# Performance work log

Hardware: AMD Instinct MI355X
Metric: run time of the kernel (lower is better)

The kernel has to match this reference:

```python
import jax, jax.numpy as jnp
import numpy as np
from jax import lax

B = 64
HW = 72           # high-res grid hardcoded in the layer
LOW = 9           # 72 / stride 8
C = 3
N_ITERS = 200     # self._iterations
W_SCALE = 0.01    # keeps the FISTA operator contractive with random weights
DN = ('NHWC', 'HWIO', 'NHWC')


def setup_inputs() -> dict:
    key = jax.random.key(0)
    k1, k2, k3, k4 = jax.random.split(key, 4)
    x = jax.random.normal(k1, (B, LOW, LOW, C), jnp.float32)
    lam = jax.random.uniform(k2, (B,), jnp.float32)            # per-sample threshold
    w_conv = jax.random.normal(k3, (40, 40, C, C), jnp.float32) * W_SCALE  # Conv2D kernel
    b_conv = jnp.zeros((C,), jnp.float32)
    w_ct = jax.random.normal(k4, (5, 5, C, C), jnp.float32) * W_SCALE      # Conv2DTranspose kernel
    b_ct = jnp.zeros((C,), jnp.float32)
    return {"x": x, "lam": lam, "w_conv": w_conv, "b_conv": b_conv,
            "w_ct": w_ct, "b_ct": b_ct}


def reference(x, lam, w_conv, b_conv, w_ct, b_ct):
    lam4 = lam[:, None, None, None]  # (B,1,1,1) per-sample soft-threshold

    def A(y):  # Conv2D(3,(40,40),strides=8,'same'): (B,72,72,3)->(B,9,9,3)
        return lax.conv_general_dilated(y, w_conv, (8, 8), 'SAME',
                                        dimension_numbers=DN) + b_conv

    def At(r):  # Conv2DTranspose(3,(5,5),strides=8,'same'): (B,9,9,3)->(B,72,72,3)
        return lax.conv_transpose(r, w_ct, (8, 8), 'SAME',
                                  dimension_numbers=DN) + b_ct

    def softthresh(w):
        return jax.nn.relu(w - lam4) - jax.nn.relu(-w - lam4)

    def step(carry, _):
        y_tmp, y_last, t = carry
        re = At(x - A(y_tmp))
        w = y_tmp - re                      # mu = 1.0
        y_new = softthresh(w)
        t_n = (1.0 + jnp.sqrt(1.0 + 4.0 * t * t)) / 2.0
        y_tmp_next = y_new + (t - 1.0) / t_n * (y_new - y_last)
        return (y_tmp_next, y_new, t_n), None

    z = jnp.zeros((x.shape[0], HW, HW, C), x.dtype)
    init = (z, z, jnp.float32(1.0))
    (_, y_new, _), _ = lax.scan(step, init, None, length=N_ITERS)
    return y_new
```

## Files before the change

kernel.cpp:

```cpp
#include <hip/hip_runtime.h>
#include <math.h>


#define ITERS 200
#define THREADS 576
#define WGOFF 0
#define WCTOFF 19200
#define APOFF 19800
#define CNTOFF 144256
#define LY 0
#define LYL 3888
#define LA 7776
#define LXS 8020
#define LWG 8264
#define LWCT 14664
#define LT 15264
#define SMEMF 20608

typedef float f32x2 __attribute__((ext_vector_type(2)));

template <int CTRL>
__device__ __forceinline__ float dpp_add(float x) {
  int moved = __builtin_amdgcn_update_dpp(0, __float_as_int(x), CTRL, 0xF, 0xF, true);
  return x + __int_as_float(moved);
}

__global__ void k0_init(const float* __restrict__ w_conv,
                        const float* __restrict__ w_ct,
                        float* __restrict__ ws) {
  const int i = blockIdx.x * 256 + threadIdx.x;
  if (i < 19200) {
    const int lane = i & 63;
    const int rest = i >> 6;
    const int g = rest / 75;
    const int tc = rest - 75 * g;
    const int t = tc / 3;
    const int co = tc - 3 * t;
    const int th = t / 5;
    const int tw = t - 5 * th;
    const int q = lane >> 4;
    const int pl = lane & 15;
    float v = 0.f;
    if (q < 3) {
      const int p = g * 16 + pl;
      const int ph = p >> 3;
      const int pw = p & 7;
      v = w_conv[(((8 * th + ph) * 40 + (8 * tw + pw)) * 3 + q) * 3 + co];
    }
    ws[WGOFF + i] = v;
  }
  if (i < 600) {
    const int c = i / 200;
    const int rem = i - 200 * c;
    float v = 0.f;
    if (rem < 192) {
      const int ci = rem >> 6;
      const int p = rem & 63;
      const int rh = p >> 3;
      const int rw = p & 7;
      if (rh < 5 && rw < 5) v = w_ct[(((4 - rh) * 5 + (4 - rw)) * 3 + ci) * 3 + c];
    }
    ws[WCTOFF + i] = v;
  }
  if (i < 4096) ((int*)ws)[CNTOFF + i] = 0;
}

__global__ __launch_bounds__(THREADS) void fista_split(
    float* __restrict__ ws,
    const float* __restrict__ x, const float* __restrict__ lam,
    const float* __restrict__ b_conv, const float* __restrict__ b_ct,
    float* __restrict__ out) {
  __shared__ __align__(16) float smem[SMEMF];
  const int tid = threadIdx.x;
  const int blk = blockIdx.x;
  const int n = blk & 63;
  const int g = blk >> 6;
  const int lane = tid & 63;
  const int wid = tid >> 6;
  const int q = lane >> 4;
  const int pl = lane & 15;
  const int ylane = ((q < 3) ? q : 2) * 16 + pl;
  const int oh = (wid == 0) ? 0 : (wid == 1) ? 4 : (wid == 4) ? 8
               : (wid == 8) ? 1 : wid;

  int* __restrict__ cnt = (int*)ws + CNTOFF + n * 64;
  const float lam_n = lam[n];
  const float bcv = b_conv[tid % 3];
  const float bct0 = b_ct[0], bct1 = b_ct[1], bct2 = b_ct[2];

  for (int i = tid; i < SMEMF; i += THREADS) smem[i] = 0.f;
  __syncthreads();
  for (int i = tid; i < 4800; i += THREADS) {
    const int lane_i = i & 63;
    const int tc = i >> 6;
    const int t_i = tc / 3;
    const int co_i = tc - 3 * t_i;
    smem[LWG + (t_i * 64 + lane_i) * 4 + co_i] = ws[WGOFF + g * 4800 + i];
  }
  for (int i = tid; i < 600; i += THREADS) smem[LWCT + i] = ws[WCTOFF + i];
  if (tid < 243) smem[LXS + tid] = x[n * 243 + tid];
  __syncthreads();

  const int idx3 = tid >> 1;
  const int cell = idx3 / 3;
  const int c = idx3 - 3 * cell;
  const int cb = 3 * cell;
  const int plb = (tid & 1) * 8;
  const int pb = g * 16 + plb;

  float t = 1.0f;
#pragma unroll 1
  for (int iter = 0; iter < ITERS; ++iter) {
    {
      f32x2 a01[9];
      float a2[9];
#pragma unroll
      for (int k = 0; k < 9; ++k) { a01[k].x = 0.f; a01[k].y = 0.f; a2[k] = 0.f; }

#pragma unroll
      for (int th = 0; th < 5; ++th) {
        const int r = oh + th - 2;
        if (r >= 0 && r <= 8) {
          f32x2 y2[9];
#pragma unroll
          for (int wc = 0; wc < 9; ++wc) {
            const float yv = smem[LY + r * 432 + wc * 48 + ylane];
            y2[wc].x = yv; y2[wc].y = yv;
          }

#pragma unroll
          for (int tw = 0; tw < 5; ++tw) {
            const float4 wv =
                *(const float4*)&smem[LWG + ((th * 5 + tw) * 64 + lane) * 4];
            f32x2 w01; w01.x = wv.x; w01.y = wv.y;
#pragma unroll
            for (int ow = 0; ow < 9; ++ow) {
              const int col = ow + tw - 2;
              if (col >= 0 && col <= 8) {
                a01[ow] += y2[col] * w01;
                a2[ow]  += y2[col].x * wv.z;
              }
            }
          }
        }
      }

      float s4[27];
#pragma unroll
      for (int k = 0; k < 27; ++k) {
        const int ow = k / 3, co = k - 3 * ow;
        const float av = (co == 0) ? a01[ow].x : (co == 1) ? a01[ow].y : a2[ow];
        const float s1 = dpp_add<0x111>(av);
        s4[k] = dpp_add<0x112>(s1);
      }
      {
        float* Tw = &smem[LT + wid * 540];
        if ((lane & 3) == 3) {
          const int m = lane >> 2;
#pragma unroll
          for (int k = 0; k < 27; ++k) Tw[k * 20 + m] = s4[k];
        }
        asm volatile("s_waitcnt lgkmcnt(0)" ::: "memory");
        if (lane < 27) {
          const float4* Tr = (const float4*)&Tw[lane * 20];
          const float4 p0 = Tr[0];
          const float4 p1 = Tr[1];
          const float4 p2 = Tr[2];
          const float4 p3 = Tr[3];
          const float s01 = (p0.x + p0.y) + (p0.z + p0.w);
          const float s23 = (p1.x + p1.y) + (p1.z + p1.w);
          const float s45 = (p2.x + p2.y) + (p2.z + p2.w);
          const float s67 = (p3.x + p3.y) + (p3.z + p3.w);
          const float s = (s01 + s23) + (s45 + s67);
          float* ap = ws + APOFF + ((((iter & 1) * 64 + n) * 4 + g) * 243)
                      + oh * 27 + lane;
          __hip_atomic_store(ap, s, __ATOMIC_RELAXED, __HIP_MEMORY_SCOPE_AGENT);
        }
      }
    }

    float4 py0 = {}, py1 = {}, pq0 = {}, pq1 = {};
    float4 w0a = {}, w0b = {}, w1a = {}, w1b = {}, w2a = {}, w2b = {};
    if (tid < 486) {
      float4* lyv  = (float4*)&smem[LY];
      float4* lylv = (float4*)&smem[LYL];
      py0 = lyv[2 * tid];  py1 = lyv[2 * tid + 1];
      pq0 = lylv[2 * tid]; pq1 = lylv[2 * tid + 1];
      w0a = *(const float4*)&smem[LWCT + c * 200 +   0 + pb];
      w0b = *(const float4*)&smem[LWCT + c * 200 +   4 + pb];
      w1a = *(const float4*)&smem[LWCT + c * 200 +  64 + pb];
      w1b = *(const float4*)&smem[LWCT + c * 200 +  68 + pb];
      w2a = *(const float4*)&smem[LWCT + c * 200 + 128 + pb];
      w2b = *(const float4*)&smem[LWCT + c * 200 + 132 + pb];
    }

    __syncthreads();
    if (tid == 0) {
      __hip_atomic_fetch_add(cnt, 1, __ATOMIC_RELAXED, __HIP_MEMORY_SCOPE_AGENT);
      const int target = 4 * (iter + 1);
      while (__hip_atomic_load(cnt, __ATOMIC_RELAXED, __HIP_MEMORY_SCOPE_AGENT)
             < target)
        __builtin_amdgcn_s_sleep(1);
    }
    __syncthreads();

    if (tid < 243) {
      const float* ap = ws + APOFF + ((iter & 1) * 64 + n) * 972;
      const float a0 = __hip_atomic_load(ap + tid, __ATOMIC_RELAXED,
                                         __HIP_MEMORY_SCOPE_AGENT);
      const float a1 = __hip_atomic_load(ap + 243 + tid, __ATOMIC_RELAXED,
                                         __HIP_MEMORY_SCOPE_AGENT);
      const float a2v = __hip_atomic_load(ap + 486 + tid, __ATOMIC_RELAXED,
                                          __HIP_MEMORY_SCOPE_AGENT);
      const float a3 = __hip_atomic_load(ap + 729 + tid, __ATOMIC_RELAXED,
                                         __HIP_MEMORY_SCOPE_AGENT);
      smem[LA + tid] = smem[LXS + tid] - (a0 + a1 + a2v + a3 + bcv);
    }
    __syncthreads();

    const float tn = (1.0f + sqrtf(1.0f + 4.0f * t * t)) * 0.5f;
    const float beta = (t - 1.0f) / tn;
    t = tn;

    const bool lastit = (iter == ITERS - 1);
    if (tid < 486) {
      const float r0  = smem[LA + cb + 0];
      const float r1  = smem[LA + cb + 1];
      const float r2v = smem[LA + cb + 2];
      const float bct = (c == 0) ? bct0 : ((c == 1) ? bct1 : bct2);

      const float wct0[8] = {w0a.x, w0a.y, w0a.z, w0a.w, w0b.x, w0b.y, w0b.z, w0b.w};
      const float wct1[8] = {w1a.x, w1a.y, w1a.z, w1a.w, w1b.x, w1b.y, w1b.z, w1b.w};
      const float wct2[8] = {w2a.x, w2a.y, w2a.z, w2a.w, w2b.x, w2b.y, w2b.z, w2b.w};
      const float yv[8]   = {py0.x, py0.y, py0.z, py0.w, py1.x, py1.y, py1.z, py1.w};
      float yn[8];
#pragma unroll
      for (int j = 0; j < 8; ++j) {
        const float re = bct + r0 * wct0[j] + r1 * wct1[j] + r2v * wct2[j];
        const float wvv = yv[j] - re;
        yn[j] = fmaxf(wvv - lam_n, 0.f) - fmaxf(-wvv - lam_n, 0.f);
      }

      float4* lyv  = (float4*)&smem[LY];
      float4* lylv = (float4*)&smem[LYL];
      if (!lastit) {
        const float ylv[8] = {pq0.x, pq0.y, pq0.z, pq0.w, pq1.x, pq1.y, pq1.z, pq1.w};
        float4 s0, s1, m0, m1;
        s0.x = yn[0]; s0.y = yn[1]; s0.z = yn[2]; s0.w = yn[3];
        s1.x = yn[4]; s1.y = yn[5]; s1.z = yn[6]; s1.w = yn[7];
        m0.x = yn[0] + beta * (yn[0] - ylv[0]);
        m0.y = yn[1] + beta * (yn[1] - ylv[1]);
        m0.z = yn[2] + beta * (yn[2] - ylv[2]);
        m0.w = yn[3] + beta * (yn[3] - ylv[3]);
        m1.x = yn[4] + beta * (yn[4] - ylv[4]);
        m1.y = yn[5] + beta * (yn[5] - ylv[5]);
        m1.z = yn[6] + beta * (yn[6] - ylv[6]);
        m1.w = yn[7] + beta * (yn[7] - ylv[7]);
        lylv[2 * tid] = s0; lylv[2 * tid + 1] = s1;
        lyv[2 * tid]  = m0; lyv[2 * tid + 1]  = m1;
      } else {
        const int part = pb >> 3;
        const int qh = cell / 9;
        const int qw = cell - 9 * qh;
        const int ih = 8 * qh + part;
        float* op = out + ((n * 72 + ih) * 72 + 8 * qw) * 3 + c;
#pragma unroll
        for (int j = 0; j < 8; ++j) op[3 * j] = yn[j];
      }
    }
    __syncthreads();
  }
}

extern "C" void kernel_launch(void* const* d_in, const int* in_sizes, int n_in,
                              void* d_out, int out_size, void* d_ws, size_t ws_size,
                              hipStream_t stream) {
  const float* x      = (const float*)d_in[0];
  const float* lam    = (const float*)d_in[1];
  const float* w_conv = (const float*)d_in[2];
  const float* b_conv = (const float*)d_in[3];
  const float* w_ct   = (const float*)d_in[4];
  const float* b_ct   = (const float*)d_in[5];
  float* out = (float*)d_out;
  float* ws  = (float*)d_ws;

  hipLaunchKernelGGL(k0_init, dim3(80), dim3(256), 0, stream, w_conv, w_ct, ws);
  hipLaunchKernelGGL(fista_split, dim3(256), dim3(THREADS), 0, stream,
                     ws, x, lam, b_conv, b_ct, out);
}
```

Baseline: 955.5 us.

## Replace counter barrier with sentinel-flagged partial buffers and split y smem layout

```diff
diff --git a/kernel.cpp b/kernel.cpp
--- a/kernel.cpp
+++ b/kernel.cpp
@@ -4,10 +4,11 @@
 
 #define ITERS 200
 #define THREADS 576
+#define SENTU 0x7FC0DEADu
 #define WGOFF 0
 #define WCTOFF 19200
 #define APOFF 19800
-#define CNTOFF 144256
+#define CNTOFF 268632
 #define LY 0
 #define LYL 3888
 #define LA 7776
@@ -62,6 +63,8 @@
     }
     ws[WCTOFF + i] = v;
   }
+  for (int j = i; j < 248832; j += 80 * 256)
+    ((unsigned*)ws)[APOFF + j] = SENTU;
   if (i < 4096) ((int*)ws)[CNTOFF + i] = 0;
 }
 
@@ -80,6 +83,7 @@
   const int q = lane >> 4;
   const int pl = lane & 15;
   const int ylane = ((q < 3) ? q : 2) * 16 + pl;
+  const int ylane2 = ((ylane >> 2) & 1) * 1944 + (ylane >> 3) * 4 + (ylane & 3);
   const int oh = (wid == 0) ? 0 : (wid == 1) ? 4 : (wid == 4) ? 8
                : (wid == 8) ? 1 : wid;
 
@@ -111,6 +115,9 @@
   float t = 1.0f;
 #pragma unroll 1
   for (int iter = 0; iter < ITERS; ++iter) {
+    int gate_seen = __hip_atomic_load(cnt, __ATOMIC_RELAXED,
+                                      __HIP_MEMORY_SCOPE_AGENT);
+
     {
       f32x2 a01[9];
       float a2[9];
@@ -124,7 +131,7 @@
           f32x2 y2[9];
 #pragma unroll
           for (int wc = 0; wc < 9; ++wc) {
-            const float yv = smem[LY + r * 432 + wc * 48 + ylane];
+            const float yv = smem[LY + r * 216 + wc * 24 + ylane2];
             y2[wc].x = yv; y2[wc].y = yv;
           }
 
@@ -160,6 +167,10 @@
 #pragma unroll
           for (int k = 0; k < 27; ++k) Tw[k * 20 + m] = s4[k];
         }
+        const int gate_target = 4 * (iter - 1);
+        while (gate_seen < gate_target)
+          gate_seen = __hip_atomic_load(cnt, __ATOMIC_RELAXED,
+                                        __HIP_MEMORY_SCOPE_AGENT);
         asm volatile("s_waitcnt lgkmcnt(0)" ::: "memory");
         if (lane < 27) {
           const float4* Tr = (const float4*)&Tw[lane * 20];
@@ -172,9 +183,15 @@
           const float s45 = (p2.x + p2.y) + (p2.z + p2.w);
           const float s67 = (p3.x + p3.y) + (p3.z + p3.w);
           const float s = (s01 + s23) + (s45 + s67);
-          float* ap = ws + APOFF + ((((iter & 1) * 64 + n) * 4 + g) * 243)
+          float* ap = ws + APOFF + (((iter & 3) * 64 + n) * 4 + g) * 243
                       + oh * 27 + lane;
           __hip_atomic_store(ap, s, __ATOMIC_RELAXED, __HIP_MEMORY_SCOPE_AGENT);
+          if (iter >= 2) {
+            unsigned* cp = (unsigned*)ws + APOFF
+                + ((((iter - 2) & 3) * 64 + n) * 4 + g) * 243 + oh * 27 + lane;
+            __hip_atomic_store(cp, SENTU, __ATOMIC_RELAXED,
+                               __HIP_MEMORY_SCOPE_AGENT);
+          }
         }
       }
     }
@@ -182,10 +199,10 @@
     float4 py0 = {}, py1 = {}, pq0 = {}, pq1 = {};
     float4 w0a = {}, w0b = {}, w1a = {}, w1b = {}, w2a = {}, w2b = {};
     if (tid < 486) {
-      float4* lyv  = (float4*)&smem[LY];
-      float4* lylv = (float4*)&smem[LYL];
-      py0 = lyv[2 * tid];  py1 = lyv[2 * tid + 1];
-      pq0 = lylv[2 * tid]; pq1 = lylv[2 * tid + 1];
+      py0 = *(const float4*)&smem[LY  + 4 * tid];
+      py1 = *(const float4*)&smem[LY  + 1944 + 4 * tid];
+      pq0 = *(const float4*)&smem[LYL + 4 * tid];
+      pq1 = *(const float4*)&smem[LYL + 1944 + 4 * tid];
       w0a = *(const float4*)&smem[LWCT + c * 200 +   0 + pb];
       w0b = *(const float4*)&smem[LWCT + c * 200 +   4 + pb];
       w1a = *(const float4*)&smem[LWCT + c * 200 +  64 + pb];
@@ -194,29 +211,29 @@
       w2b = *(const float4*)&smem[LWCT + c * 200 + 132 + pb];
     }
 
+    if (tid < 243) {
+      const unsigned* apb = (const unsigned*)ws + APOFF
+                            + ((iter & 3) * 64 + n) * 972;
+      unsigned u0, u1, u2, u3;
+      do {
+        u0 = __hip_atomic_load(apb + tid,       __ATOMIC_RELAXED,
+                               __HIP_MEMORY_SCOPE_AGENT);
+        u1 = __hip_atomic_load(apb + 243 + tid, __ATOMIC_RELAXED,
+                               __HIP_MEMORY_SCOPE_AGENT);
+        u2 = __hip_atomic_load(apb + 486 + tid, __ATOMIC_RELAXED,
+                               __HIP_MEMORY_SCOPE_AGENT);
+        u3 = __hip_atomic_load(apb + 729 + tid, __ATOMIC_RELAXED,
+                               __HIP_MEMORY_SCOPE_AGENT);
+      } while ((u0 == SENTU) | (u1 == SENTU) | (u2 == SENTU) | (u3 == SENTU));
+      const float a0  = __uint_as_float(u0);
+      const float a1  = __uint_as_float(u1);
+      const float a2v = __uint_as_float(u2);
+      const float a3  = __uint_as_float(u3);
+      smem[LA + tid] = smem[LXS + tid] - (a0 + a1 + a2v + a3 + bcv);
+    }
     __syncthreads();
-    if (tid == 0) {
+    if (tid == 0)
       __hip_atomic_fetch_add(cnt, 1, __ATOMIC_RELAXED, __HIP_MEMORY_SCOPE_AGENT);
-      const int target = 4 * (iter + 1);
-      while (__hip_atomic_load(cnt, __ATOMIC_RELAXED, __HIP_MEMORY_SCOPE_AGENT)
-             < target)
-        __builtin_amdgcn_s_sleep(1);
-    }
-    __syncthreads();
-
-    if (tid < 243) {
-      const float* ap = ws + APOFF + ((iter & 1) * 64 + n) * 972;
-      const float a0 = __hip_atomic_load(ap + tid, __ATOMIC_RELAXED,
-                                         __HIP_MEMORY_SCOPE_AGENT);
-      const float a1 = __hip_atomic_load(ap + 243 + tid, __ATOMIC_RELAXED,
-                                         __HIP_MEMORY_SCOPE_AGENT);
-      const float a2v = __hip_atomic_load(ap + 486 + tid, __ATOMIC_RELAXED,
-                                          __HIP_MEMORY_SCOPE_AGENT);
-      const float a3 = __hip_atomic_load(ap + 729 + tid, __ATOMIC_RELAXED,
-                                         __HIP_MEMORY_SCOPE_AGENT);
-      smem[LA + tid] = smem[LXS + tid] - (a0 + a1 + a2v + a3 + bcv);
-    }
-    __syncthreads();
 
     const float tn = (1.0f + sqrtf(1.0f + 4.0f * t * t)) * 0.5f;
     const float beta = (t - 1.0f) / tn;
@@ -241,8 +258,6 @@
         yn[j] = fmaxf(wvv - lam_n, 0.f) - fmaxf(-wvv - lam_n, 0.f);
       }
 
-      float4* lyv  = (float4*)&smem[LY];
-      float4* lylv = (float4*)&smem[LYL];
       if (!lastit) {
         const float ylv[8] = {pq0.x, pq0.y, pq0.z, pq0.w, pq1.x, pq1.y, pq1.z, pq1.w};
         float4 s0, s1, m0, m1;
@@ -256,8 +271,10 @@
         m1.y = yn[5] + beta * (yn[5] - ylv[5]);
         m1.z = yn[6] + beta * (yn[6] - ylv[6]);
         m1.w = yn[7] + beta * (yn[7] - ylv[7]);
-        lylv[2 * tid] = s0; lylv[2 * tid + 1] = s1;
-        lyv[2 * tid]  = m0; lyv[2 * tid + 1]  = m1;
+        *(float4*)&smem[LYL + 4 * tid] = s0;
+        *(float4*)&smem[LYL + 1944 + 4 * tid] = s1;
+        *(float4*)&smem[LY  + 4 * tid] = m0;
+        *(float4*)&smem[LY  + 1944 + 4 * tid] = m1;
       } else {
         const int part = pb >> 3;
         const int qh = cell / 9;
```

Measured after the change: 965.1 us. About the same (+1.0%).

## Process two samples per block to overlap cross-block barrier with compute

Applied to the files above, without the earlier changes.

```diff
diff --git a/kernel.cpp b/kernel.cpp
--- a/kernel.cpp
+++ b/kernel.cpp
@@ -8,14 +8,18 @@
 #define WCTOFF 19200
 #define APOFF 19800
 #define CNTOFF 144256
-#define LY 0
-#define LYL 3888
-#define LA 7776
-#define LXS 8020
-#define LWG 8264
-#define LWCT 14664
-#define LT 15264
-#define SMEMF 20608
+#define LWG 0
+#define LWCT 6400
+#define LT 7000
+#define LYA 11860
+#define LYLA 15748
+#define LAA 19636
+#define LXSA 19880
+#define LYB 20124
+#define LYLB 24012
+#define LAB 27900
+#define LXSB 28144
+#define SMEMF 28388
 
 typedef float f32x2 __attribute__((ext_vector_type(2)));
 
@@ -65,6 +69,152 @@
   if (i < 4096) ((int*)ws)[CNTOFF + i] = 0;
 }
 
+
+__device__ __forceinline__ void stage1_one(
+    float* smem, float* ws, int LYbase, int n, int g, int iter,
+    int oh, int lane, int wid, int ylane) {
+  f32x2 a01[9];
+  float a2[9];
+#pragma unroll
+  for (int k = 0; k < 9; ++k) { a01[k].x = 0.f; a01[k].y = 0.f; a2[k] = 0.f; }
+
+#pragma unroll
+  for (int th = 0; th < 5; ++th) {
+    const int r = oh + th - 2;
+    if (r >= 0 && r <= 8) {
+      f32x2 y2[9];
+#pragma unroll
+      for (int wc = 0; wc < 9; ++wc) {
+        const float yv = smem[LYbase + r * 432 + wc * 48 + ylane];
+        y2[wc].x = yv; y2[wc].y = yv;
+      }
+#pragma unroll
+      for (int tw = 0; tw < 5; ++tw) {
+        const float4 wv =
+            *(const float4*)&smem[LWG + ((th * 5 + tw) * 64 + lane) * 4];
+        f32x2 w01; w01.x = wv.x; w01.y = wv.y;
+#pragma unroll
+        for (int ow = 0; ow < 9; ++ow) {
+          const int col = ow + tw - 2;
+          if (col >= 0 && col <= 8) {
+            a01[ow] += y2[col] * w01;
+            a2[ow]  += y2[col].x * wv.z;
+          }
+        }
+      }
+    }
+  }
+
+  float s4[27];
+#pragma unroll
+  for (int k = 0; k < 27; ++k) {
+    const int ow = k / 3, co = k - 3 * ow;
+    const float av = (co == 0) ? a01[ow].x : (co == 1) ? a01[ow].y : a2[ow];
+    const float s1 = dpp_add<0x111>(av);
+    s4[k] = dpp_add<0x112>(s1);
+  }
+  float* Tw = &smem[LT + wid * 540];
+  if ((lane & 3) == 3) {
+    const int m = lane >> 2;
+#pragma unroll
+    for (int k = 0; k < 27; ++k) Tw[k * 20 + m] = s4[k];
+  }
+  asm volatile("s_waitcnt lgkmcnt(0)" ::: "memory");
+  if (lane < 27) {
+    const float4* Tr = (const float4*)&Tw[lane * 20];
+    const float4 p0 = Tr[0];
+    const float4 p1 = Tr[1];
+    const float4 p2 = Tr[2];
+    const float4 p3 = Tr[3];
+    const float s01 = (p0.x + p0.y) + (p0.z + p0.w);
+    const float s23 = (p1.x + p1.y) + (p1.z + p1.w);
+    const float s45 = (p2.x + p2.y) + (p2.z + p2.w);
+    const float s67 = (p3.x + p3.y) + (p3.z + p3.w);
+    const float s = (s01 + s23) + (s45 + s67);
+    float* ap = ws + APOFF + ((iter & 1) * 64 + n) * 972 + g * 243
+                + oh * 27 + lane;
+    __hip_atomic_store(ap, s, __ATOMIC_RELAXED, __HIP_MEMORY_SCOPE_AGENT);
+  }
+}
+
+__device__ __forceinline__ void prepass_one(
+    float* smem, const float* ws, int LAb, int LXSb, int n, int iter,
+    int tid, float bcv) {
+  if (tid < 243) {
+    const float* ap = ws + APOFF + ((iter & 1) * 64 + n) * 972;
+    const float a0 = __hip_atomic_load(ap + tid, __ATOMIC_RELAXED,
+                                       __HIP_MEMORY_SCOPE_AGENT);
+    const float a1 = __hip_atomic_load(ap + 243 + tid, __ATOMIC_RELAXED,
+                                       __HIP_MEMORY_SCOPE_AGENT);
+    const float a2v = __hip_atomic_load(ap + 486 + tid, __ATOMIC_RELAXED,
+                                        __HIP_MEMORY_SCOPE_AGENT);
+    const float a3 = __hip_atomic_load(ap + 729 + tid, __ATOMIC_RELAXED,
+                                       __HIP_MEMORY_SCOPE_AGENT);
+    smem[LAb + tid] = smem[LXSb + tid] - (a0 + a1 + a2v + a3 + bcv);
+  }
+}
+
+__device__ __forceinline__ void stage2_one(
+    float* smem, int LYb, int LYLb, int LAb, int tid, int cell, int c,
+    int cb, int pb, float lam_n, float bct, float beta, bool lastit,
+    float* out, int n) {
+  if (tid < 486) {
+    const float r0  = smem[LAb + cb + 0];
+    const float r1  = smem[LAb + cb + 1];
+    const float r2v = smem[LAb + cb + 2];
+
+    const float4 w0a = *(const float4*)&smem[LWCT + c * 200 +   0 + pb];
+    const float4 w0b = *(const float4*)&smem[LWCT + c * 200 +   4 + pb];
+    const float4 w1a = *(const float4*)&smem[LWCT + c * 200 +  64 + pb];
+    const float4 w1b = *(const float4*)&smem[LWCT + c * 200 +  68 + pb];
+    const float4 w2a = *(const float4*)&smem[LWCT + c * 200 + 128 + pb];
+    const float4 w2b = *(const float4*)&smem[LWCT + c * 200 + 132 + pb];
+    const float wct0[8] = {w0a.x, w0a.y, w0a.z, w0a.w, w0b.x, w0b.y, w0b.z, w0b.w};
+    const float wct1[8] = {w1a.x, w1a.y, w1a.z, w1a.w, w1b.x, w1b.y, w1b.z, w1b.w};
+    const float wct2[8] = {w2a.x, w2a.y, w2a.z, w2a.w, w2b.x, w2b.y, w2b.z, w2b.w};
+
+    float4* lyv  = (float4*)&smem[LYb];
+    float4* lylv = (float4*)&smem[LYLb];
+    const float4 y0 = lyv[2 * tid];
+    const float4 y1 = lyv[2 * tid + 1];
+    const float yv[8] = {y0.x, y0.y, y0.z, y0.w, y1.x, y1.y, y1.z, y1.w};
+    float yn[8];
+#pragma unroll
+    for (int j = 0; j < 8; ++j) {
+      const float re = bct + r0 * wct0[j] + r1 * wct1[j] + r2v * wct2[j];
+      const float wvv = yv[j] - re;
+      yn[j] = fmaxf(wvv - lam_n, 0.f) - fmaxf(-wvv - lam_n, 0.f);
+    }
+
+    if (!lastit) {
+      const float4 l0 = lylv[2 * tid];
+      const float4 l1 = lylv[2 * tid + 1];
+      const float ylv[8] = {l0.x, l0.y, l0.z, l0.w, l1.x, l1.y, l1.z, l1.w};
+      float4 s0, s1, m0, m1;
+      s0.x = yn[0]; s0.y = yn[1]; s0.z = yn[2]; s0.w = yn[3];
+      s1.x = yn[4]; s1.y = yn[5]; s1.z = yn[6]; s1.w = yn[7];
+      m0.x = yn[0] + beta * (yn[0] - ylv[0]);
+      m0.y = yn[1] + beta * (yn[1] - ylv[1]);
+      m0.z = yn[2] + beta * (yn[2] - ylv[2]);
+      m0.w = yn[3] + beta * (yn[3] - ylv[3]);
+      m1.x = yn[4] + beta * (yn[4] - ylv[4]);
+      m1.y = yn[5] + beta * (yn[5] - ylv[5]);
+      m1.z = yn[6] + beta * (yn[6] - ylv[6]);
+      m1.w = yn[7] + beta * (yn[7] - ylv[7]);
+      lylv[2 * tid] = s0; lylv[2 * tid + 1] = s1;
+      lyv[2 * tid]  = m0; lyv[2 * tid + 1]  = m1;
+    } else {
+      const int part = pb >> 3;
+      const int qh = cell / 9;
+      const int qw = cell - 9 * qh;
+      const int ih = 8 * qh + part;
+      float* op = out + ((n * 72 + ih) * 72 + 8 * qw) * 3 + c;
+#pragma unroll
+      for (int j = 0; j < 8; ++j) op[3 * j] = yn[j];
+    }
+  }
+}
+
 __global__ __launch_bounds__(THREADS) void fista_split(
     float* __restrict__ ws,
     const float* __restrict__ x, const float* __restrict__ lam,
@@ -72,9 +222,10 @@
     float* __restrict__ out) {
   __shared__ __align__(16) float smem[SMEMF];
   const int tid = threadIdx.x;
-  const int blk = blockIdx.x;
-  const int n = blk & 63;
-  const int g = blk >> 6;
+  const int b = blockIdx.x;
+  const int g = b >> 5;
+  const int nA = b & 31;
+  const int nB = 32 + (b & 31);
   const int lane = tid & 63;
   const int wid = tid >> 6;
   const int q = lane >> 4;
@@ -83,8 +234,10 @@
   const int oh = (wid == 0) ? 0 : (wid == 1) ? 4 : (wid == 4) ? 8
                : (wid == 8) ? 1 : wid;
 
-  int* __restrict__ cnt = (int*)ws + CNTOFF + n * 64;
-  const float lam_n = lam[n];
+  int* __restrict__ cntA = (int*)ws + CNTOFF + nA * 64;
+  int* __restrict__ cntB = (int*)ws + CNTOFF + nB * 64;
+  const float lamA = lam[nA];
+  const float lamB = lam[nB];
   const float bcv = b_conv[tid % 3];
   const float bct0 = b_ct[0], bct1 = b_ct[1], bct2 = b_ct[2];
 
@@ -98,7 +251,10 @@
     smem[LWG + (t_i * 64 + lane_i) * 4 + co_i] = ws[WGOFF + g * 4800 + i];
   }
   for (int i = tid; i < 600; i += THREADS) smem[LWCT + i] = ws[WCTOFF + i];
-  if (tid < 243) smem[LXS + tid] = x[n * 243 + tid];
+  if (tid < 243) {
+    smem[LXSA + tid] = x[nA * 243 + tid];
+    smem[LXSB + tid] = x[nB * 243 + tid];
+  }
   __syncthreads();
 
   const int idx3 = tid >> 1;
@@ -107,167 +263,51 @@
   const int cb = 3 * cell;
   const int plb = (tid & 1) * 8;
   const int pb = g * 16 + plb;
+  const float bct = (c == 0) ? bct0 : ((c == 1) ? bct1 : bct2);
 
   float t = 1.0f;
 #pragma unroll 1
   for (int iter = 0; iter < ITERS; ++iter) {
-    {
-      f32x2 a01[9];
-      float a2[9];
-#pragma unroll
-      for (int k = 0; k < 9; ++k) { a01[k].x = 0.f; a01[k].y = 0.f; a2[k] = 0.f; }
-
-#pragma unroll
-      for (int th = 0; th < 5; ++th) {
-        const int r = oh + th - 2;
-        if (r >= 0 && r <= 8) {
-          f32x2 y2[9];
-#pragma unroll
-          for (int wc = 0; wc < 9; ++wc) {
-            const float yv = smem[LY + r * 432 + wc * 48 + ylane];
-            y2[wc].x = yv; y2[wc].y = yv;
-          }
-
-#pragma unroll
-          for (int tw = 0; tw < 5; ++tw) {
-            const float4 wv =
-                *(const float4*)&smem[LWG + ((th * 5 + tw) * 64 + lane) * 4];
-            f32x2 w01; w01.x = wv.x; w01.y = wv.y;
-#pragma unroll
-            for (int ow = 0; ow < 9; ++ow) {
-              const int col = ow + tw - 2;
-              if (col >= 0 && col <= 8) {
-                a01[ow] += y2[col] * w01;
-                a2[ow]  += y2[col].x * wv.z;
-              }
-            }
-          }
-        }
-      }
-
-      float s4[27];
-#pragma unroll
-      for (int k = 0; k < 27; ++k) {
-        const int ow = k / 3, co = k - 3 * ow;
-        const float av = (co == 0) ? a01[ow].x : (co == 1) ? a01[ow].y : a2[ow];
-        const float s1 = dpp_add<0x111>(av);
-        s4[k] = dpp_add<0x112>(s1);
-      }
-      {
-        float* Tw = &smem[LT + wid * 540];
-        if ((lane & 3) == 3) {
-          const int m = lane >> 2;
-#pragma unroll
-          for (int k = 0; k < 27; ++k) Tw[k * 20 + m] = s4[k];
-        }
-        asm volatile("s_waitcnt lgkmcnt(0)" ::: "memory");
-        if (lane < 27) {
-          const float4* Tr = (const float4*)&Tw[lane * 20];
-          const float4 p0 = Tr[0];
-          const float4 p1 = Tr[1];
-          const float4 p2 = Tr[2];
-          const float4 p3 = Tr[3];
-          const float s01 = (p0.x + p0.y) + (p0.z + p0.w);
-          const float s23 = (p1.x + p1.y) + (p1.z + p1.w);
-          const float s45 = (p2.x + p2.y) + (p2.z + p2.w);
-          const float s67 = (p3.x + p3.y) + (p3.z + p3.w);
-          const float s = (s01 + s23) + (s45 + s67);
-          float* ap = ws + APOFF + ((((iter & 1) * 64 + n) * 4 + g) * 243)
-                      + oh * 27 + lane;
-          __hip_atomic_store(ap, s, __ATOMIC_RELAXED, __HIP_MEMORY_SCOPE_AGENT);
-        }
-      }
-    }
-
-    float4 py0 = {}, py1 = {}, pq0 = {}, pq1 = {};
-    float4 w0a = {}, w0b = {}, w1a = {}, w1b = {}, w2a = {}, w2b = {};
-    if (tid < 486) {
-      float4* lyv  = (float4*)&smem[LY];
-      float4* lylv = (float4*)&smem[LYL];
-      py0 = lyv[2 * tid];  py1 = lyv[2 * tid + 1];
-      pq0 = lylv[2 * tid]; pq1 = lylv[2 * tid + 1];
-      w0a = *(const float4*)&smem[LWCT + c * 200 +   0 + pb];
-      w0b = *(const float4*)&smem[LWCT + c * 200 +   4 + pb];
-      w1a = *(const float4*)&smem[LWCT + c * 200 +  64 + pb];
-      w1b = *(const float4*)&smem[LWCT + c * 200 +  68 + pb];
-      w2a = *(const float4*)&smem[LWCT + c * 200 + 128 + pb];
-      w2b = *(const float4*)&smem[LWCT + c * 200 + 132 + pb];
-    }
-
+    const bool lastit = (iter == ITERS - 1);
+
+    stage1_one(smem, ws, LYA, nA, g, iter, oh, lane, wid, ylane);
+    __syncthreads();
+    if (tid == 0)
+      __hip_atomic_fetch_add(cntA, 1, __ATOMIC_RELAXED, __HIP_MEMORY_SCOPE_AGENT);
+
+    stage1_one(smem, ws, LYB, nB, g, iter, oh, lane, wid, ylane);
     __syncthreads();
     if (tid == 0) {
-      __hip_atomic_fetch_add(cnt, 1, __ATOMIC_RELAXED, __HIP_MEMORY_SCOPE_AGENT);
+      __hip_atomic_fetch_add(cntB, 1, __ATOMIC_RELAXED, __HIP_MEMORY_SCOPE_AGENT);
       const int target = 4 * (iter + 1);
-      while (__hip_atomic_load(cnt, __ATOMIC_RELAXED, __HIP_MEMORY_SCOPE_AGENT)
+      while (__hip_atomic_load(cntA, __ATOMIC_RELAXED, __HIP_MEMORY_SCOPE_AGENT)
              < target)
         __builtin_amdgcn_s_sleep(1);
     }
     __syncthreads();
 
-    if (tid < 243) {
-      const float* ap = ws + APOFF + ((iter & 1) * 64 + n) * 972;
-      const float a0 = __hip_atomic_load(ap + tid, __ATOMIC_RELAXED,
-                                         __HIP_MEMORY_SCOPE_AGENT);
-      const float a1 = __hip_atomic_load(ap + 243 + tid, __ATOMIC_RELAXED,
-                                         __HIP_MEMORY_SCOPE_AGENT);
-      const float a2v = __hip_atomic_load(ap + 486 + tid, __ATOMIC_RELAXED,
-                                          __HIP_MEMORY_SCOPE_AGENT);
-      const float a3 = __hip_atomic_load(ap + 729 + tid, __ATOMIC_RELAXED,
-                                         __HIP_MEMORY_SCOPE_AGENT);
-      smem[LA + tid] = smem[LXS + tid] - (a0 + a1 + a2v + a3 + bcv);
-    }
+    prepass_one(smem, ws, LAA, LXSA, nA, iter, tid, bcv);
     __syncthreads();
 
     const float tn = (1.0f + sqrtf(1.0f + 4.0f * t * t)) * 0.5f;
     const float beta = (t - 1.0f) / tn;
     t = tn;
 
-    const bool lastit = (iter == ITERS - 1);
-    if (tid < 486) {
-      const float r0  = smem[LA + cb + 0];
-      const float r1  = smem[LA + cb + 1];
-      const float r2v = smem[LA + cb + 2];
-      const float bct = (c == 0) ? bct0 : ((c == 1) ? bct1 : bct2);
-
-      const float wct0[8] = {w0a.x, w0a.y, w0a.z, w0a.w, w0b.x, w0b.y, w0b.z, w0b.w};
-      const float wct1[8] = {w1a.x, w1a.y, w1a.z, w1a.w, w1b.x, w1b.y, w1b.z, w1b.w};
-      const float wct2[8] = {w2a.x, w2a.y, w2a.z, w2a.w, w2b.x, w2b.y, w2b.z, w2b.w};
-      const float yv[8]   = {py0.x, py0.y, py0.z, py0.w, py1.x, py1.y, py1.z, py1.w};
-      float yn[8];
-#pragma unroll
-      for (int j = 0; j < 8; ++j) {
-        const float re = bct + r0 * wct0[j] + r1 * wct1[j] + r2v * wct2[j];
-        const float wvv = yv[j] - re;
-        yn[j] = fmaxf(wvv - lam_n, 0.f) - fmaxf(-wvv - lam_n, 0.f);
-      }
-
-      float4* lyv  = (float4*)&smem[LY];
-      float4* lylv = (float4*)&smem[LYL];
-      if (!lastit) {
-        const float ylv[8] = {pq0.x, pq0.y, pq0.z, pq0.w, pq1.x, pq1.y, pq1.z, pq1.w};
-        float4 s0, s1, m0, m1;
-        s0.x = yn[0]; s0.y = yn[1]; s0.z = yn[2]; s0.w = yn[3];
-        s1.x = yn[4]; s1.y = yn[5]; s1.z = yn[6]; s1.w = yn[7];
-        m0.x = yn[0] + beta * (yn[0] - ylv[0]);
-        m0.y = yn[1] + beta * (yn[1] - ylv[1]);
-        m0.z = yn[2] + beta * (yn[2] - ylv[2]);
-        m0.w = yn[3] + beta * (yn[3] - ylv[3]);
-        m1.x = yn[4] + beta * (yn[4] - ylv[4]);
-        m1.y = yn[5] + beta * (yn[5] - ylv[5]);
-        m1.z = yn[6] + beta * (yn[6] - ylv[6]);
-        m1.w = yn[7] + beta * (yn[7] - ylv[7]);
-        lylv[2 * tid] = s0; lylv[2 * tid + 1] = s1;
-        lyv[2 * tid]  = m0; lyv[2 * tid + 1]  = m1;
-      } else {
-        const int part = pb >> 3;
-        const int qh = cell / 9;
-        const int qw = cell - 9 * qh;
-        const int ih = 8 * qh + part;
-        float* op = out + ((n * 72 + ih) * 72 + 8 * qw) * 3 + c;
-#pragma unroll
-        for (int j = 0; j < 8; ++j) op[3 * j] = yn[j];
-      }
-    }
+    stage2_one(smem, LYA, LYLA, LAA, tid, cell, c, cb, pb, lamA, bct, beta,
+               lastit, out, nA);
+    __syncthreads();
+
+    if (tid == 0) {
+      const int target = 4 * (iter + 1);
+      while (__hip_atomic_load(cntB, __ATOMIC_RELAXED, __HIP_MEMORY_SCOPE_AGENT)
+             < target)
+        __builtin_amdgcn_s_sleep(1);
+    }
+    __syncthreads();
+    prepass_one(smem, ws, LAB, LXSB, nB, iter, tid, bcv);
+    __syncthreads();
+    stage2_one(smem, LYB, LYLB, LAB, tid, cell, c, cb, pb, lamB, bct, beta,
+               lastit, out, nB);
     __syncthreads();
   }
 }
@@ -285,6 +325,6 @@
   float* ws  = (float*)d_ws;
 
   hipLaunchKernelGGL(k0_init, dim3(80), dim3(256), 0, stream, w_conv, w_ct, ws);
-  hipLaunchKernelGGL(fista_split, dim3(256), dim3(THREADS), 0, stream,
+  hipLaunchKernelGGL(fista_split, dim3(128), dim3(THREADS), 0, stream,
                      ws, x, lam, b_conv, b_ct, out);
 }
```

Measured after the change: 1.662 ms. 1.74x slower.
